# Performance work log

Measured on AMD Instinct MI355X. Metric: run time of the kernel, lower is better.

Reference implementation:

```python
import jax, jax.numpy as jnp
import numpy as np

B_SZ, L, H, P, V, OUT_LEN = 32, 4096, 512, 384, 32, 16
DT_MIN, DT_MAX = 0.001, 0.1


def setup_inputs() -> dict:
    key = jax.random.key(0)
    ks = jax.random.split(key, 12)
    tokens = jax.random.randint(ks[0], (B_SZ, L), 0, V, dtype=jnp.int32)
    embed = jax.random.normal(ks[1], (V, H), dtype=jnp.float32) * 0.02
    # S5 diagonal state: Lambda = Lambda_re + i*Lambda_im (stable: Re < 0)
    Lambda_re = -0.5 * jax.random.uniform(ks[2], (P,), dtype=jnp.float32) - 1e-3
    Lambda_im = jnp.pi * jnp.arange(P, dtype=jnp.float32)
    B_re = jax.random.normal(ks[3], (P, H), dtype=jnp.float32) / np.sqrt(H)
    B_im = jax.random.normal(ks[4], (P, H), dtype=jnp.float32) / np.sqrt(H)
    C_re = jax.random.normal(ks[5], (H, P), dtype=jnp.float32) / np.sqrt(P)
    C_im = jax.random.normal(ks[6], (H, P), dtype=jnp.float32) / np.sqrt(P)
    D = jax.random.normal(ks[7], (H,), dtype=jnp.float32)
    log_step = jax.random.uniform(
        ks[8], (P,), dtype=jnp.float32,
        minval=np.log(DT_MIN), maxval=np.log(DT_MAX))
    W1 = jax.random.normal(ks[9], (H, H), dtype=jnp.float32) / np.sqrt(H)
    b1 = jnp.zeros((H,), dtype=jnp.float32)
    W2 = jax.random.normal(ks[10], (H, V), dtype=jnp.float32) / np.sqrt(H)
    b2 = jnp.zeros((V,), dtype=jnp.float32)
    return dict(tokens=tokens, embed=embed, Lambda_re=Lambda_re,
                Lambda_im=Lambda_im, B_re=B_re, B_im=B_im, C_re=C_re,
                C_im=C_im, D=D, log_step=log_step, W1=W1, b1=b1, W2=W2, b2=b2)


def _s5_scan(Lbar, Bu_bar):
    # Lbar: (P,) complex; Bu_bar: (B,L,P) complex
    A = jnp.broadcast_to(Lbar, Bu_bar.shape)

    def comb(e1, e2):
        A1, b1 = e1
        A2, b2 = e2
        return A2 * A1, A2 * b1 + b2

    _, xs = jax.lax.associative_scan(comb, (A, Bu_bar), axis=1)
    return xs  # (B,L,P) hidden states


def reference(tokens, embed, Lambda_re, Lambda_im, B_re, B_im,
              C_re, C_im, D, log_step, W1, b1, W2, b2):
    u = embed[tokens]                              # (B,L,H) real
    Lam = Lambda_re + 1j * Lambda_im               # (P,)
    step = jnp.exp(log_step)                       # (P,)
    Lbar = jnp.exp(Lam * step)                     # ZOH: exp(Lambda*dt)
    Bc = B_re + 1j * B_im                          # (P,H)
    Cc = C_re + 1j * C_im                          # (H,P)
    Bu = jnp.einsum('blh,ph->blp', u, Bc)          # (B,L,P) complex
    Bu_bar = ((Lbar - 1.0) / Lam) * Bu             # ZOH input discretization
    xs = _s5_scan(Lbar, Bu_bar)                    # (B,L,P)
    # conj_sym=True -> 2 * Re(C x) + D u
    y = 2.0 * jnp.einsum('blp,hp->blh', xs, Cc).real + u * D
    y = y[:, -OUT_LEN:, :]                         # (B,16,H)
    h = jax.nn.relu(y @ W1 + b1)
    return h @ W2 + b2                             # (B,16,V)
```

## Files before the change

### kernel.cpp

```cpp
#include <hip/hip_runtime.h>

#define B_SZ 32
#define L 4096
#define H 512
#define P 384
#define V 32
#define OUT_LEN 16
#define NC 16
#define CHUNK 255
#define T0 4080

#define OFF_DBL   0
#define OFF_LBARF 4608
#define OFF_M     5376
#define OFF_CT    29952
#define OFF_PART  423168
#define OFF_XS    816384
#define OFF_YT    1209600
#define OFF_HP    29952

__global__ __launch_bounds__(256) void k_init(
    const float* __restrict__ Lre, const float* __restrict__ Lim,
    const float* __restrict__ log_step,
    const float* __restrict__ Cre, const float* __restrict__ Cim,
    float* __restrict__ ws)
{
    int bx = blockIdx.x, tid = threadIdx.x;
    if (bx < 192) {
        __shared__ float sre[32][33], sim[32][33];
        int tp = bx >> 4, th = bx & 15;
        int col = tid & 31, r0 = tid >> 5;
        #pragma unroll
        for (int it = 0; it < 4; ++it) {
            int row = r0 + 8 * it;
            int h = th * 32 + row, p = tp * 32 + col;
            sre[col][row] = Cre[h * P + p];
            sim[col][row] = Cim[h * P + p];
        }
        __syncthreads();
        #pragma unroll
        for (int it = 0; it < 4; ++it) {
            int pl = r0 + 8 * it;
            int p = tp * 32 + pl, h = th * 32 + col;
            ws[OFF_CT + (2 * p) * H + h]     = sre[pl][col];
            ws[OFF_CT + (2 * p + 1) * H + h] = sim[pl][col];
        }
    } else {
        int p = (bx - 192) * 256 + tid;
        if (p >= P) return;
        double dstep = exp((double)log_step[p]);
        double are = (double)Lre[p] * dstep, aim = (double)Lim[p] * dstep;
        double mag = exp(are);
        double lbr = mag * cos(aim), lbi = mag * sin(aim);
        double wmag = exp((double)CHUNK * are);
        double wang = (double)CHUNK * aim;
        double wr = wmag * cos(wang), wi = wmag * sin(wang);
        double lre = (double)Lre[p], lim = (double)Lim[p];
        double nr = lbr - 1.0, ni = lbi;
        double den = lre * lre + lim * lim;
        double cr = (nr * lre + ni * lim) / den, ci = (ni * lre - nr * lim) / den;
        double* d = (double*)ws + p * 6;
        d[0] = lbr; d[1] = lbi; d[2] = wr; d[3] = wi; d[4] = cr; d[5] = ci;
        ws[OFF_LBARF + 2 * p]     = (float)lbr;
        ws[OFF_LBARF + 2 * p + 1] = (float)lbi;
    }
}

__global__ __launch_bounds__(256) void k_mtab(
    const float* __restrict__ embed, const float* __restrict__ Bre,
    const float* __restrict__ Bim, float* __restrict__ ws)
{
    int wid = blockIdx.x * 4 + (threadIdx.x >> 6);
    int lane = threadIdx.x & 63;
    int v = wid / P, p = wid - v * P;
    const float4* ev = (const float4*)(embed + v * H) + lane * 2;
    const float4* br = (const float4*)(Bre + p * H) + lane * 2;
    const float4* bi = (const float4*)(Bim + p * H) + lane * 2;
    float dr = 0.f, di = 0.f;
    #pragma unroll
    for (int q = 0; q < 2; ++q) {
        float4 e = ev[q], r = br[q], i = bi[q];
        dr += r.x * e.x + r.y * e.y + r.z * e.z + r.w * e.w;
        di += i.x * e.x + i.y * e.y + i.z * e.z + i.w * e.w;
    }
    #pragma unroll
    for (int off = 32; off; off >>= 1) {
        dr += __shfl_down(dr, off);
        di += __shfl_down(di, off);
    }
    if (lane == 0) {
        const double* d = (const double*)ws + p * 6;
        double cr = d[4], ci = d[5];
        double mr = cr * (double)dr - ci * (double)di;
        double mi = cr * (double)di + ci * (double)dr;
        ws[OFF_M + (v * P + p) * 2]     = (float)mr;
        ws[OFF_M + (v * P + p) * 2 + 1] = (float)mi;
    }
}

__global__ __launch_bounds__(192) void k_scan(
    const int* __restrict__ tokens, const float* __restrict__ ws,
    float* __restrict__ part)
{
    __shared__ float2 sM[V * 193];
    int x = blockIdx.x, b = blockIdx.y;
    int c = x >> 1, ph = x & 1;
    int tid = threadIdx.x;
    const float2* Mg = (const float2*)(ws + OFF_M);
    #pragma unroll
    for (int v = 0; v < V; ++v)
        sM[v * 193 + tid] = Mg[v * P + ph * 192 + tid];
    int p = ph * 192 + tid;
    float Lr = ws[OFF_LBARF + 2 * p], Li = ws[OFF_LBARF + 2 * p + 1];
    __syncthreads();
    float ar = 0.f, ai = 0.f;
    const int* tk = tokens + b * L + c * CHUNK;
    #pragma unroll 3
    for (int i = 0; i < CHUNK; ++i) {
        int t = tk[i];
        float2 m = sM[t * 193 + tid];
        float nar = fmaf(Lr, ar, fmaf(-Li, ai, m.x));
        float nai = fmaf(Lr, ai, fmaf( Li, ar, m.y));
        ar = nar; ai = nai;
    }
    float* pt = part + ((b * NC + c) * P + p) * 2;
    pt[0] = ar; pt[1] = ai;
}

__global__ __launch_bounds__(256) void k_combine(
    const int* __restrict__ tokens, float* __restrict__ ws)
{
    int id = blockIdx.x * 256 + threadIdx.x;
    int b = id / P, p = id - b * P;
    const double* d = (const double*)ws + p * 6;
    double lbr = d[0], lbi = d[1], wr = d[2], wi = d[3];
    double xr = 0.0, xi = 0.0;
    const float* pp = ws + OFF_PART + (b * NC * P + p) * 2;
    #pragma unroll
    for (int c = 0; c < NC; ++c) {
        double pr = (double)pp[c * P * 2], pi = (double)pp[c * P * 2 + 1];
        double tr = wr * xr - wi * xi + pr;
        double ti = wr * xi + wi * xr + pi;
        xr = tr; xi = ti;
    }
    const float* M = ws + OFF_M;
    float* xs = ws + OFF_XS + (b * P + p) * OUT_LEN * 2;
    const int* tk = tokens + b * L + T0;
    #pragma unroll
    for (int j = 0; j < OUT_LEN; ++j) {
        int t = tk[j];
        double mr = (double)M[(t * P + p) * 2], mi = (double)M[(t * P + p) * 2 + 1];
        double tr = lbr * xr - lbi * xi + mr;
        double ti = lbr * xi + lbi * xr + mi;
        xr = tr; xi = ti;
        xs[2 * j] = (float)xr; xs[2 * j + 1] = (float)xi;
    }
}

__global__ __launch_bounds__(256) void k_y(
    const int* __restrict__ tokens, const float* __restrict__ embed,
    const float* __restrict__ D, float* __restrict__ ws)
{
    __shared__ float sxs[384 * 16];
    __shared__ float sred[4 * 64 * 9];
    int x = blockIdx.x, b = blockIdx.y;
    int lh = x & 1, hq = x >> 1;
    int tid = threadIdx.x;
    int h0 = hq * 64;

    {
        const float4* src = (const float4*)(ws + OFF_XS);
        float4* dst = (float4*)sxs;
        #pragma unroll
        for (int it = 0; it < 6; ++it) {
            int f = tid + 256 * it;
            int p = f >> 2, q = f & 3;
            dst[f] = src[(b * P + p) * 8 + lh * 4 + q];
        }
    }
    __syncthreads();

    int hl = tid & 63, pg = tid >> 6;
    int h = h0 + hl;
    const float* ct = ws + OFF_CT;
    float acc[8];
    #pragma unroll
    for (int i = 0; i < 8; ++i) acc[i] = 0.f;

    int p0 = pg * 96;
    #pragma unroll 2
    for (int pp = 0; pp < 96; ++pp) {
        int p = p0 + pp;
        float cre = ct[(2 * p) * H + h];
        float cim = ct[(2 * p + 1) * H + h];
        const float4* xv = (const float4*)(sxs + p * 16);
        float4 x0 = xv[0], x1 = xv[1], x2 = xv[2], x3 = xv[3];
        acc[0] = fmaf(cre, x0.x, fmaf(-cim, x0.y, acc[0]));
        acc[1] = fmaf(cre, x0.z, fmaf(-cim, x0.w, acc[1]));
        acc[2] = fmaf(cre, x1.x, fmaf(-cim, x1.y, acc[2]));
        acc[3] = fmaf(cre, x1.z, fmaf(-cim, x1.w, acc[3]));
        acc[4] = fmaf(cre, x2.x, fmaf(-cim, x2.y, acc[4]));
        acc[5] = fmaf(cre, x2.z, fmaf(-cim, x2.w, acc[5]));
        acc[6] = fmaf(cre, x3.x, fmaf(-cim, x3.y, acc[6]));
        acc[7] = fmaf(cre, x3.z, fmaf(-cim, x3.w, acc[7]));
    }
    #pragma unroll
    for (int i = 0; i < 8; ++i)
        sred[(pg * 64 + hl) * 9 + i] = acc[i];
    __syncthreads();

    #pragma unroll
    for (int oo = 0; oo < 2; ++oo) {
        int o = tid + 256 * oo;
        int ohl = o & 63, oi = o >> 6;
        float s = sred[ohl * 9 + oi] + sred[(64 + ohl) * 9 + oi]
                + sred[(128 + ohl) * 9 + oi] + sred[(192 + ohl) * 9 + oi];
        int l = lh * 8 + oi;
        int t = tokens[b * L + T0 + l];
        int hh = h0 + ohl;
        ws[OFF_YT + (b * OUT_LEN + l) * H + hh] =
            2.f * s + embed[t * H + hh] * D[hh];
    }
}

__global__ __launch_bounds__(256) void k_fc1(
    const float* __restrict__ W1, const float* __restrict__ ws,
    float* __restrict__ hp)
{
    __shared__ float ys[128 * 8];
    int bx = blockIdx.x;
    int rg = bx >> 3, jh = (bx >> 2) & 1, kc = bx & 3;
    int tid = threadIdx.x;
    int j = jh * 256 + tid;
    int r0 = rg * 8, k0 = kc * 128;
    const float* yt = ws + OFF_YT;

    int kk = tid & 127, rr = tid >> 7;
    #pragma unroll
    for (int it = 0; it < 4; ++it)
        ys[kk * 8 + rr + 2 * it] = yt[(r0 + rr + 2 * it) * H + k0 + kk];
    __syncthreads();

    const float* wp = W1 + k0 * H + j;
    float w0 = wp[0], w1 = wp[H];
    float acc[8] = {0, 0, 0, 0, 0, 0, 0, 0};
    for (int k = 0; k < 128; k += 2) {
        float a0 = w0, a1 = w1;
        if (k + 2 < 128) { w0 = wp[(k + 2) * H]; w1 = wp[(k + 3) * H]; }
        const float4* y0 = (const float4*)(ys + k * 8);
        float4 p0 = y0[0], p1 = y0[1], p2 = y0[2], p3 = y0[3];
        acc[0] = fmaf(p0.x, a0, acc[0]);
        acc[1] = fmaf(p0.y, a0, acc[1]);
        acc[2] = fmaf(p0.z, a0, acc[2]);
        acc[3] = fmaf(p0.w, a0, acc[3]);
        acc[4] = fmaf(p1.x, a0, acc[4]);
        acc[5] = fmaf(p1.y, a0, acc[5]);
        acc[6] = fmaf(p1.z, a0, acc[6]);
        acc[7] = fmaf(p1.w, a0, acc[7]);
        acc[0] = fmaf(p2.x, a1, acc[0]);
        acc[1] = fmaf(p2.y, a1, acc[1]);
        acc[2] = fmaf(p2.z, a1, acc[2]);
        acc[3] = fmaf(p2.w, a1, acc[3]);
        acc[4] = fmaf(p3.x, a1, acc[4]);
        acc[5] = fmaf(p3.y, a1, acc[5]);
        acc[6] = fmaf(p3.z, a1, acc[6]);
        acc[7] = fmaf(p3.w, a1, acc[7]);
    }
    #pragma unroll
    for (int i = 0; i < 8; ++i)
        hp[(kc * 512 + r0 + i) * H + j] = acc[i];
}

__global__ __launch_bounds__(256) void k_fc2(
    const float* __restrict__ b1, const float* __restrict__ W2,
    const float* __restrict__ b2, const float* __restrict__ hp,
    float* __restrict__ out)
{
    __shared__ float sh[512];
    __shared__ float red[8 * 32];
    int r = blockIdx.x, tid = threadIdx.x;
    #pragma unroll
    for (int half = 0; half < 2; ++half) {
        int j = half * 256 + tid;
        float s = b1[j] + hp[r * H + j] + hp[(512 + r) * H + j]
                        + hp[(1024 + r) * H + j] + hp[(1536 + r) * H + j];
        sh[j] = fmaxf(s, 0.f);
    }
    __syncthreads();
    int seg = tid >> 5, o = tid & 31;
    float acc = 0.f;
    const float* w2 = W2 + seg * 64 * V + o;
    const float* hv = sh + seg * 64;
    #pragma unroll 4
    for (int jj = 0; jj < 64; ++jj)
        acc = fmaf(hv[jj], w2[jj * V], acc);
    red[seg * 32 + o] = acc;
    __syncthreads();
    if (tid < 32) {
        float s = b2[tid];
        #pragma unroll
        for (int ss = 0; ss < 8; ++ss) s += red[ss * 32 + tid];
        out[r * V + tid] = s;
    }
}

extern "C" void kernel_launch(void* const* d_in, const int* in_sizes, int n_in,
                              void* d_out, int out_size, void* d_ws, size_t ws_size,
                              hipStream_t stream)
{
    const int*   tokens = (const int*)d_in[0];
    const float* embed  = (const float*)d_in[1];
    const float* Lre    = (const float*)d_in[2];
    const float* Lim    = (const float*)d_in[3];
    const float* Bre    = (const float*)d_in[4];
    const float* Bim    = (const float*)d_in[5];
    const float* Cre    = (const float*)d_in[6];
    const float* Cim    = (const float*)d_in[7];
    const float* D      = (const float*)d_in[8];
    const float* lstep  = (const float*)d_in[9];
    const float* W1     = (const float*)d_in[10];
    const float* b1     = (const float*)d_in[11];
    const float* W2     = (const float*)d_in[12];
    const float* b2     = (const float*)d_in[13];
    float* out = (float*)d_out;
    float* ws  = (float*)d_ws;

    k_init   <<<194, 256, 0, stream>>>(Lre, Lim, lstep, Cre, Cim, ws);
    k_mtab   <<<3072, 256, 0, stream>>>(embed, Bre, Bim, ws);
    k_scan   <<<dim3(32, 32), 192, 0, stream>>>(tokens, ws, ws + OFF_PART);
    k_combine<<<48, 256, 0, stream>>>(tokens, ws);
    k_y      <<<dim3(16, 32), 256, 0, stream>>>(tokens, embed, D, ws);
    k_fc1    <<<512, 256, 0, stream>>>(W1, ws, ws + OFF_HP);
    k_fc2    <<<512, 256, 0, stream>>>(b1, W2, b2, ws + OFF_HP, out);
}
```

Baseline: 164.9 us.

## Fuse prep kernels, fold chunk combine into y kernel, defer ZOH scaling

Merges k_init and k_mtab into a single prep launch, with the M table now holding raw B·embed products. The ZOH coefficient multiply moves to after the scan, applied per state in k_y. The chunk combine and the last-16-step recurrence now run inside k_y, with 384 threads, one per state. This removes two launches and the xs round trip through global memory. In exchange, every k_y block redoes the combine for its batch, 16 times redundantly. fc1 and fc2 inner loops are also restructured with deeper W1 prefetch and split accumulators.

```diff
diff --git a/kernel.cpp b/kernel.cpp
--- a/kernel.cpp
+++ b/kernel.cpp
@@ -13,40 +13,24 @@
 #define OFF_DBL   0
 #define OFF_LBARF 4608
 #define OFF_M     5376
+#define OFF_CT    423168
+#undef  OFF_CT
 #define OFF_CT    29952
 #define OFF_PART  423168
-#define OFF_XS    816384
-#define OFF_YT    1209600
-#define OFF_HP    29952
-
-__global__ __launch_bounds__(256) void k_init(
+#define OFF_YT    816384
+#define OFF_HP    1078528
+
+__global__ __launch_bounds__(256) void k_prep(
+    const float* __restrict__ embed, const float* __restrict__ Bre,
+    const float* __restrict__ Bim,
     const float* __restrict__ Lre, const float* __restrict__ Lim,
     const float* __restrict__ log_step,
     const float* __restrict__ Cre, const float* __restrict__ Cim,
     float* __restrict__ ws)
 {
     int bx = blockIdx.x, tid = threadIdx.x;
-    if (bx < 192) {
-        __shared__ float sre[32][33], sim[32][33];
-        int tp = bx >> 4, th = bx & 15;
-        int col = tid & 31, r0 = tid >> 5;
-        #pragma unroll
-        for (int it = 0; it < 4; ++it) {
-            int row = r0 + 8 * it;
-            int h = th * 32 + row, p = tp * 32 + col;
-            sre[col][row] = Cre[h * P + p];
-            sim[col][row] = Cim[h * P + p];
-        }
-        __syncthreads();
-        #pragma unroll
-        for (int it = 0; it < 4; ++it) {
-            int pl = r0 + 8 * it;
-            int p = tp * 32 + pl, h = th * 32 + col;
-            ws[OFF_CT + (2 * p) * H + h]     = sre[pl][col];
-            ws[OFF_CT + (2 * p + 1) * H + h] = sim[pl][col];
-        }
-    } else {
-        int p = (bx - 192) * 256 + tid;
+    if (bx < 2) {
+        int p = bx * 256 + tid;
         if (p >= P) return;
         double dstep = exp((double)log_step[p]);
         double are = (double)Lre[p] * dstep, aim = (double)Lim[p] * dstep;
@@ -63,38 +47,49 @@
         d[0] = lbr; d[1] = lbi; d[2] = wr; d[3] = wi; d[4] = cr; d[5] = ci;
         ws[OFF_LBARF + 2 * p]     = (float)lbr;
         ws[OFF_LBARF + 2 * p + 1] = (float)lbi;
-    }
-}
-
-__global__ __launch_bounds__(256) void k_mtab(
-    const float* __restrict__ embed, const float* __restrict__ Bre,
-    const float* __restrict__ Bim, float* __restrict__ ws)
-{
-    int wid = blockIdx.x * 4 + (threadIdx.x >> 6);
-    int lane = threadIdx.x & 63;
-    int v = wid / P, p = wid - v * P;
-    const float4* ev = (const float4*)(embed + v * H) + lane * 2;
-    const float4* br = (const float4*)(Bre + p * H) + lane * 2;
-    const float4* bi = (const float4*)(Bim + p * H) + lane * 2;
-    float dr = 0.f, di = 0.f;
-    #pragma unroll
-    for (int q = 0; q < 2; ++q) {
-        float4 e = ev[q], r = br[q], i = bi[q];
-        dr += r.x * e.x + r.y * e.y + r.z * e.z + r.w * e.w;
-        di += i.x * e.x + i.y * e.y + i.z * e.z + i.w * e.w;
-    }
-    #pragma unroll
-    for (int off = 32; off; off >>= 1) {
-        dr += __shfl_down(dr, off);
-        di += __shfl_down(di, off);
-    }
-    if (lane == 0) {
-        const double* d = (const double*)ws + p * 6;
-        double cr = d[4], ci = d[5];
-        double mr = cr * (double)dr - ci * (double)di;
-        double mi = cr * (double)di + ci * (double)dr;
-        ws[OFF_M + (v * P + p) * 2]     = (float)mr;
-        ws[OFF_M + (v * P + p) * 2 + 1] = (float)mi;
+    } else if (bx < 194) {
+        __shared__ float sre[32][33], sim[32][33];
+        int bxx = bx - 2;
+        int tp = bxx >> 4, th = bxx & 15;
+        int col = tid & 31, r0 = tid >> 5;
+        #pragma unroll
+        for (int it = 0; it < 4; ++it) {
+            int row = r0 + 8 * it;
+            int h = th * 32 + row, p = tp * 32 + col;
+            sre[col][row] = Cre[h * P + p];
+            sim[col][row] = Cim[h * P + p];
+        }
+        __syncthreads();
+        #pragma unroll
+        for (int it = 0; it < 4; ++it) {
+            int pl = r0 + 8 * it;
+            int p = tp * 32 + pl, h = th * 32 + col;
+            ws[OFF_CT + (2 * p) * H + h]     = sre[pl][col];
+            ws[OFF_CT + (2 * p + 1) * H + h] = sim[pl][col];
+        }
+    } else {
+        int wid = (bx - 194) * 4 + (tid >> 6);
+        int lane = tid & 63;
+        int v = wid / P, p = wid - v * P;
+        const float4* ev = (const float4*)(embed + v * H) + lane * 2;
+        const float4* br = (const float4*)(Bre + p * H) + lane * 2;
+        const float4* bi = (const float4*)(Bim + p * H) + lane * 2;
+        float dr = 0.f, di = 0.f;
+        #pragma unroll
+        for (int q = 0; q < 2; ++q) {
+            float4 e = ev[q], r = br[q], i = bi[q];
+            dr += r.x * e.x + r.y * e.y + r.z * e.z + r.w * e.w;
+            di += i.x * e.x + i.y * e.y + i.z * e.z + i.w * e.w;
+        }
+        #pragma unroll
+        for (int off = 32; off; off >>= 1) {
+            dr += __shfl_down(dr, off);
+            di += __shfl_down(di, off);
+        }
+        if (lane == 0) {
+            ws[OFF_M + (v * P + p) * 2]     = dr;
+            ws[OFF_M + (v * P + p) * 2 + 1] = di;
+        }
     }
 }
 
@@ -127,55 +122,45 @@
     pt[0] = ar; pt[1] = ai;
 }
 
-__global__ __launch_bounds__(256) void k_combine(
-    const int* __restrict__ tokens, float* __restrict__ ws)
-{
-    int id = blockIdx.x * 256 + threadIdx.x;
-    int b = id / P, p = id - b * P;
-    const double* d = (const double*)ws + p * 6;
-    double lbr = d[0], lbi = d[1], wr = d[2], wi = d[3];
-    double xr = 0.0, xi = 0.0;
-    const float* pp = ws + OFF_PART + (b * NC * P + p) * 2;
-    #pragma unroll
-    for (int c = 0; c < NC; ++c) {
-        double pr = (double)pp[c * P * 2], pi = (double)pp[c * P * 2 + 1];
-        double tr = wr * xr - wi * xi + pr;
-        double ti = wr * xi + wi * xr + pi;
-        xr = tr; xi = ti;
-    }
-    const float* M = ws + OFF_M;
-    float* xs = ws + OFF_XS + (b * P + p) * OUT_LEN * 2;
-    const int* tk = tokens + b * L + T0;
-    #pragma unroll
-    for (int j = 0; j < OUT_LEN; ++j) {
-        int t = tk[j];
-        double mr = (double)M[(t * P + p) * 2], mi = (double)M[(t * P + p) * 2 + 1];
-        double tr = lbr * xr - lbi * xi + mr;
-        double ti = lbr * xi + lbi * xr + mi;
-        xr = tr; xi = ti;
-        xs[2 * j] = (float)xr; xs[2 * j + 1] = (float)xi;
-    }
-}
-
-__global__ __launch_bounds__(256) void k_y(
+__global__ __launch_bounds__(384) void k_y(
     const int* __restrict__ tokens, const float* __restrict__ embed,
     const float* __restrict__ D, float* __restrict__ ws)
 {
-    __shared__ float sxs[384 * 16];
-    __shared__ float sred[4 * 64 * 9];
+    __shared__ float sxs[P * 16];
+    __shared__ float sred[384 * 9];
     int x = blockIdx.x, b = blockIdx.y;
     int lh = x & 1, hq = x >> 1;
     int tid = threadIdx.x;
     int h0 = hq * 64;
 
     {
-        const float4* src = (const float4*)(ws + OFF_XS);
-        float4* dst = (float4*)sxs;
-        #pragma unroll
-        for (int it = 0; it < 6; ++it) {
-            int f = tid + 256 * it;
-            int p = f >> 2, q = f & 3;
-            dst[f] = src[(b * P + p) * 8 + lh * 4 + q];
+        int p = tid;
+        const double* d = (const double*)ws + p * 6;
+        double lbr = d[0], lbi = d[1], wr = d[2], wi = d[3], cr = d[4], ci = d[5];
+        double zr = 0.0, zi = 0.0;
+        const float* pp = ws + OFF_PART + (b * NC * P + p) * 2;
+        #pragma unroll
+        for (int c = 0; c < NC; ++c) {
+            double pr = (double)pp[c * P * 2], pi = (double)pp[c * P * 2 + 1];
+            double tr = wr * zr - wi * zi + pr;
+            double ti = wr * zi + wi * zr + pi;
+            zr = tr; zi = ti;
+        }
+        const float* M0 = ws + OFF_M;
+        const int* tk = tokens + b * L + T0;
+        #pragma unroll
+        for (int j = 0; j < OUT_LEN; ++j) {
+            int t = tk[j];
+            double mr = (double)M0[(t * P + p) * 2];
+            double mi = (double)M0[(t * P + p) * 2 + 1];
+            double tr = lbr * zr - lbi * zi + mr;
+            double ti = lbr * zi + lbi * zr + mi;
+            zr = tr; zi = ti;
+            if ((j >> 3) == lh) {
+                int jj = j & 7;
+                sxs[p * 16 + 2 * jj]     = (float)(cr * zr - ci * zi);
+                sxs[p * 16 + 2 * jj + 1] = (float)(cr * zi + ci * zr);
+            }
         }
     }
     __syncthreads();
@@ -186,11 +171,10 @@
     float acc[8];
     #pragma unroll
     for (int i = 0; i < 8; ++i) acc[i] = 0.f;
-
-    int p0 = pg * 96;
+    int p0 = pg * 64;
     #pragma unroll 2
-    for (int pp = 0; pp < 96; ++pp) {
-        int p = p0 + pp;
+    for (int ppp = 0; ppp < 64; ++ppp) {
+        int p = p0 + ppp;
         float cre = ct[(2 * p) * H + h];
         float cim = ct[(2 * p + 1) * H + h];
         const float4* xv = (const float4*)(sxs + p * 16);
@@ -211,15 +195,19 @@
 
     #pragma unroll
     for (int oo = 0; oo < 2; ++oo) {
-        int o = tid + 256 * oo;
-        int ohl = o & 63, oi = o >> 6;
-        float s = sred[ohl * 9 + oi] + sred[(64 + ohl) * 9 + oi]
-                + sred[(128 + ohl) * 9 + oi] + sred[(192 + ohl) * 9 + oi];
-        int l = lh * 8 + oi;
-        int t = tokens[b * L + T0 + l];
-        int hh = h0 + ohl;
-        ws[OFF_YT + (b * OUT_LEN + l) * H + hh] =
-            2.f * s + embed[t * H + hh] * D[hh];
+        int o = tid + 384 * oo;
+        if (o < 512) {
+            int ohl = o & 63, oi = o >> 6;
+            float s = 0.f;
+            #pragma unroll
+            for (int g = 0; g < 6; ++g)
+                s += sred[(g * 64 + ohl) * 9 + oi];
+            int l = lh * 8 + oi;
+            int t = tokens[b * L + T0 + l];
+            int hh = h0 + ohl;
+            ws[OFF_YT + (b * OUT_LEN + l) * H + hh] =
+                2.f * s + embed[t * H + hh] * D[hh];
+        }
     }
 }
 
@@ -242,29 +230,32 @@
     __syncthreads();
 
     const float* wp = W1 + k0 * H + j;
-    float w0 = wp[0], w1 = wp[H];
+    float wreg[8];
+    #pragma unroll
+    for (int u = 0; u < 8; ++u) wreg[u] = wp[u * H];
     float acc[8] = {0, 0, 0, 0, 0, 0, 0, 0};
-    for (int k = 0; k < 128; k += 2) {
-        float a0 = w0, a1 = w1;
-        if (k + 2 < 128) { w0 = wp[(k + 2) * H]; w1 = wp[(k + 3) * H]; }
-        const float4* y0 = (const float4*)(ys + k * 8);
-        float4 p0 = y0[0], p1 = y0[1], p2 = y0[2], p3 = y0[3];
-        acc[0] = fmaf(p0.x, a0, acc[0]);
-        acc[1] = fmaf(p0.y, a0, acc[1]);
-        acc[2] = fmaf(p0.z, a0, acc[2]);
-        acc[3] = fmaf(p0.w, a0, acc[3]);
-        acc[4] = fmaf(p1.x, a0, acc[4]);
-        acc[5] = fmaf(p1.y, a0, acc[5]);
-        acc[6] = fmaf(p1.z, a0, acc[6]);
-        acc[7] = fmaf(p1.w, a0, acc[7]);
-        acc[0] = fmaf(p2.x, a1, acc[0]);
-        acc[1] = fmaf(p2.y, a1, acc[1]);
-        acc[2] = fmaf(p2.z, a1, acc[2]);
-        acc[3] = fmaf(p2.w, a1, acc[3]);
-        acc[4] = fmaf(p3.x, a1, acc[4]);
-        acc[5] = fmaf(p3.y, a1, acc[5]);
-        acc[6] = fmaf(p3.z, a1, acc[6]);
-        acc[7] = fmaf(p3.w, a1, acc[7]);
+    for (int kb = 0; kb < 128; kb += 8) {
+        float cur[8];
+        #pragma unroll
+        for (int u = 0; u < 8; ++u) cur[u] = wreg[u];
+        if (kb + 8 < 128) {
+            #pragma unroll
+            for (int u = 0; u < 8; ++u) wreg[u] = wp[(kb + 8 + u) * H];
+        }
+        #pragma unroll
+        for (int u = 0; u < 8; ++u) {
+            const float4* y0 = (const float4*)(ys + (kb + u) * 8);
+            float4 p0 = y0[0], p1 = y0[1];
+            float a = cur[u];
+            acc[0] = fmaf(p0.x, a, acc[0]);
+            acc[1] = fmaf(p0.y, a, acc[1]);
+            acc[2] = fmaf(p0.z, a, acc[2]);
+            acc[3] = fmaf(p0.w, a, acc[3]);
+            acc[4] = fmaf(p1.x, a, acc[4]);
+            acc[5] = fmaf(p1.y, a, acc[5]);
+            acc[6] = fmaf(p1.z, a, acc[6]);
+            acc[7] = fmaf(p1.w, a, acc[7]);
+        }
     }
     #pragma unroll
     for (int i = 0; i < 8; ++i)
@@ -288,13 +279,17 @@
     }
     __syncthreads();
     int seg = tid >> 5, o = tid & 31;
-    float acc = 0.f;
     const float* w2 = W2 + seg * 64 * V + o;
     const float* hv = sh + seg * 64;
-    #pragma unroll 4
-    for (int jj = 0; jj < 64; ++jj)
-        acc = fmaf(hv[jj], w2[jj * V], acc);
-    red[seg * 32 + o] = acc;
+    float a0 = 0.f, a1 = 0.f, a2 = 0.f, a3 = 0.f;
+    #pragma unroll
+    for (int q = 0; q < 16; ++q) {
+        a0 = fmaf(hv[q],      w2[q * V],        a0);
+        a1 = fmaf(hv[16 + q], w2[(16 + q) * V], a1);
+        a2 = fmaf(hv[32 + q], w2[(32 + q) * V], a2);
+        a3 = fmaf(hv[48 + q], w2[(48 + q) * V], a3);
+    }
+    red[seg * 32 + o] = (a0 + a1) + (a2 + a3);
     __syncthreads();
     if (tid < 32) {
         float s = b2[tid];
@@ -325,11 +320,9 @@
     float* out = (float*)d_out;
     float* ws  = (float*)d_ws;
 
-    k_init   <<<194, 256, 0, stream>>>(Lre, Lim, lstep, Cre, Cim, ws);
-    k_mtab   <<<3072, 256, 0, stream>>>(embed, Bre, Bim, ws);
-    k_scan   <<<dim3(32, 32), 192, 0, stream>>>(tokens, ws, ws + OFF_PART);
-    k_combine<<<48, 256, 0, stream>>>(tokens, ws);
-    k_y      <<<dim3(16, 32), 256, 0, stream>>>(tokens, embed, D, ws);
-    k_fc1    <<<512, 256, 0, stream>>>(W1, ws, ws + OFF_HP);
-    k_fc2    <<<512, 256, 0, stream>>>(b1, W2, b2, ws + OFF_HP, out);
-}
+    k_prep <<<3266, 256, 0, stream>>>(embed, Bre, Bim, Lre, Lim, lstep, Cre, Cim, ws);
+    k_scan <<<dim3(32, 32), 192, 0, stream>>>(tokens, ws, ws + OFF_PART);
+    k_y    <<<dim3(16, 32), 384, 0, stream>>>(tokens, embed, D, ws);
+    k_fc1  <<<512, 256, 0, stream>>>(W1, ws, ws + OFF_HP);
+    k_fc2  <<<512, 256, 0, stream>>>(b1, W2, b2, ws + OFF_HP, out);
+}
```

Result: faster. 144.8 us (-12.2%).
